# Kernel optimization log

Measured on AMD Instinct MI355X. Metric: run time of the kernel, lower is better.

Reference implementation:

```python
import jax, jax.numpy as jnp
import numpy as np

DIM = 256
HID = DIM * 16

def setup_inputs() -> dict:
    key = jax.random.key(0)
    ks = jax.random.split(key, 6)
    B, L = 4, 2048
    x = jax.random.normal(ks[0], (B, L, DIM), dtype=jnp.float32)
    # nn.Linear(dim, hidden): weight [H, D], bias [H]
    WB = jax.random.normal(ks[1], (HID, DIM), dtype=jnp.float32) / np.sqrt(DIM)
    bB = jax.random.normal(ks[2], (HID,), dtype=jnp.float32) * 0.01
    # nn.Linear(hidden, dim): weight [D, H], bias [D]
    WC = jax.random.normal(ks[3], (DIM, HID), dtype=jnp.float32) / np.sqrt(HID)
    bC = jax.random.normal(ks[4], (DIM,), dtype=jnp.float32) * 0.01
    A = jax.random.normal(ks[5], (HID,), dtype=jnp.float32)
    return {"x": x, "WB": WB, "bB": bB, "WC": WC, "bC": bC, "A": A}

def reference(x, WB, bB, WC, bC, A):
    # b = B(x): [B, L, H]
    b = jnp.einsum('bld,hd->blh', x, WB) + bB
    a = jax.nn.sigmoid(A)  # [H], time-invariant decay
    # h_t = a * h_{t-1} + b_t  (h_0 from zero state) -> associative scan over L
    a_seq = jnp.broadcast_to(a, b.shape)
    def comb(c1, c2):
        a1, u1 = c1
        a2, u2 = c2
        return (a1 * a2, a2 * u1 + u2)
    _, h = jax.lax.associative_scan(comb, (a_seq, b), axis=1)  # [B, L, H]
    # C(h): [B, L, D]
    return jnp.einsum('blh,dh->bld', h, WC) + bC
```

## Files before the change

### kernel.cpp

```cpp
#include <hip/hip_runtime.h>
#include <hip/hip_bf16.h>

#define DIMSZ 256
#define HID 4096
#define BATCH 4
#define SEQ 2048
#define NCH 64
#define CLEN 32
#define SPLITK2 4
#define KCHUNK (HID / SPLITK2)
#define BM2 64

typedef __bf16 bf16_t;
typedef __bf16 bf16x8 __attribute__((ext_vector_type(8)));
typedef float  f32x4  __attribute__((ext_vector_type(4)));

__device__ __forceinline__ float sigmoidf_dev(float x) {
    return 1.0f / (1.0f + __expf(-x));
}

__device__ __forceinline__ void load_lds16(const bf16_t* g, bf16_t* l) {
    __builtin_amdgcn_global_load_lds(
        (const __attribute__((address_space(1))) void*)g,
        (__attribute__((address_space(3))) void*)l,
        16, 0, 0);
}

__device__ __forceinline__ bf16x8 cvt8(const float* p) {
    bf16x8 o;
    #pragma unroll
    for (int j = 0; j < 8; j++) o[j] = (bf16_t)p[j];
    return o;
}

__global__ void prep_kernel(const float* __restrict__ x,
                            const float* __restrict__ WB,
                            const float* __restrict__ WC,
                            bf16_t* __restrict__ xt,
                            bf16_t* __restrict__ WBt,
                            bf16_t* __restrict__ Wt) {
    int i = blockIdx.x * blockDim.x + threadIdx.x;
    if (i < 262144) {
        int lane = i & 63, m16 = (i >> 6) & 511, ks = i >> 15;
        int row = m16 * 16 + (lane & 15);
        int k   = ks * 32 + (lane >> 4) * 8;
        *(bf16x8*)&xt[(size_t)i * 8] = cvt8(&x[(size_t)row * DIMSZ + k]);
    } else if (i < 393216) {
        int j = i - 262144;
        int lane = j & 63, n16 = (j >> 6) & 255, ks = j >> 14;
        int row = n16 * 16 + (lane & 15);
        int k   = ks * 32 + (lane >> 4) * 8;
        *(bf16x8*)&WBt[(size_t)j * 8] = cvt8(&WB[(size_t)row * DIMSZ + k]);
    } else {
        int j = i - 393216;
        int lane = j & 63, g = (j >> 6) & 15, ks = j >> 10;
        int row = g * 16 + (lane & 15);
        int k   = ks * 32 + (lane >> 4) * 8;
        *(bf16x8*)&Wt[(size_t)j * 8] = cvt8(&WC[(size_t)row * HID + k]);
    }
}

__global__ __launch_bounds__(256)
void gemm1_fused(const bf16_t* __restrict__ xt, const bf16_t* __restrict__ WBt,
                 const float* __restrict__ bias, const float* __restrict__ Adecay,
                 bf16_t* __restrict__ Cg, float* __restrict__ totals)
{
    constexpr int N = HID;
    constexpr int LDTILE = 136;
    __shared__ bf16_t tile[128 * LDTILE];

    const int tid = threadIdx.x, wave = tid >> 6, lane = tid & 63;
    const int wm = wave >> 1, wn = wave & 1, q = lane >> 4, r16 = lane & 15;
    const int mBase = blockIdx.x * 128, nBase = blockIdx.y * 128;
    const int m16Base = blockIdx.x * 8 + wm * 4;
    const int n16Base = blockIdx.y * 8 + wn * 4;

    f32x4 acc[4][4] = {};

    #pragma unroll 2
    for (int ks = 0; ks < 8; ks++) {
        bf16x8 af[4], bfr[4];
        #pragma unroll
        for (int mt = 0; mt < 4; mt++)
            af[mt] = *(const bf16x8*)&xt[(((size_t)ks * 512 + m16Base + mt) * 64 + lane) * 8];
        #pragma unroll
        for (int nt = 0; nt < 4; nt++)
            bfr[nt] = *(const bf16x8*)&WBt[(((size_t)ks * 256 + n16Base + nt) * 64 + lane) * 8];
        #pragma unroll
        for (int mt = 0; mt < 4; mt++)
            #pragma unroll
            for (int nt = 0; nt < 4; nt++)
                acc[mt][nt] = __builtin_amdgcn_mfma_f32_16x16x32_bf16(
                    af[mt], bfr[nt], acc[mt][nt], 0, 0, 0);
    }

    #pragma unroll
    for (int nt = 0; nt < 4; nt++) {
        const int chl = wn * 64 + nt * 16 + r16;
        const float bv = bias[nBase + chl];
        #pragma unroll
        for (int mt = 0; mt < 4; mt++) {
            const int t0 = wm * 64 + mt * 16 + q * 4;
            #pragma unroll
            for (int rg = 0; rg < 4; rg++)
                tile[(t0 + rg) * LDTILE + chl] = (bf16_t)(acc[mt][nt][rg] + bv);
        }
    }
    __syncthreads();

    #pragma unroll
    for (int p = 0; p < 8; p++) {
        const int t = p * 16 + (tid >> 4);
        const int ch8 = (tid & 15) << 3;
        *(bf16x8*)&Cg[(size_t)(mBase + t) * N + nBase + ch8] =
            *(const bf16x8*)&tile[t * LDTILE + ch8];
    }

    #pragma unroll
    for (int t = 0; t < 2; t++) {
        int task = tid + t * 256;
        int ch = task & 127, ck = task >> 7;
        float a = sigmoidf_dev(Adecay[nBase + ch]);
        float v[CLEN];
        #pragma unroll
        for (int i = 0; i < CLEN; i++)
            v[i] = (float)tile[(ck * CLEN + i) * LDTILE + ch];
        float tot = 0.f;
        #pragma unroll
        for (int i = 0; i < CLEN; i++)
            tot = a * tot + v[i];
        int batch = mBase >> 11;
        int cg = ((mBase & 2047) >> 5) + ck;
        totals[(size_t)(batch * NCH + cg) * HID + nBase + ch] = tot;
    }
}

__global__ void scan_carries_kernel(const float* __restrict__ totals,
                                    const float* __restrict__ Adecay,
                                    float* __restrict__ carries)
{
    int gid = blockIdx.x * 64 + threadIdx.x;
    int ch    = gid & (HID - 1);
    int batch = gid >> 12;
    float a = sigmoidf_dev(Adecay[ch]);
    float aC = a;
    #pragma unroll
    for (int i = 0; i < 5; i++) aC *= aC;

    float v[NCH];
    #pragma unroll
    for (int c = 0; c < NCH; c++)
        v[c] = totals[(size_t)(batch * NCH + c) * HID + ch];

    float carry = 0.f;
    #pragma unroll
    for (int c = 0; c < NCH; c++) {
        carries[(size_t)(batch * NCH + c) * HID + ch] = carry;
        carry = aC * carry + v[c];
    }
}

__global__ __launch_bounds__(256)
void gemm2_fused(const bf16_t* __restrict__ bv, const bf16_t* __restrict__ Wt,
                 const float* __restrict__ Adecay, const float* __restrict__ carries,
                 bf16_t* __restrict__ P)
{
    constexpr int CKSTRIDE = BM2 * 32 + 32;
    __shared__ bf16_t hs[16896];

    const int tid = threadIdx.x, wave = tid >> 6, lane = tid & 63;
    const int q = lane >> 4, r16 = lane & 15;
    const int mBase = blockIdx.x * BM2;
    const int kBase = blockIdx.y * KCHUNK;
    const int batch = mBase >> 11;
    const int chunk0 = (mBase & 2047) >> 5;

    f32x4 acc[4][4] = {};

    for (int s = 0; s < KCHUNK / 256; s++) {
        const int chSlab = kBase + s * 256;

        if (s > 0) __syncthreads();

        #pragma unroll
        for (int i = 0; i < 8; i++) {
            int ck = wave * 2 + (i >> 2);
            int g  = i & 3;
            load_lds16(&bv[(size_t)(mBase + g * 16 + (lane >> 2)) * HID
                           + chSlab + ck * 32 + ((lane & 3) << 3)],
                       &hs[ck * CKSTRIDE + g * 512]);
        }

        const int ck = tid >> 5, ch = tid & 31;
        const int c = chSlab + ck * 32 + ch;
        const float a = sigmoidf_dev(Adecay[c]);
        float st0 = carries[(size_t)(batch * NCH + chunk0) * HID + c];
        float st1 = carries[(size_t)(batch * NCH + chunk0 + 1) * HID + c];

        __syncthreads();

        {
            bf16_t* hp = &hs[ck * CKSTRIDE + ch];
            float v[BM2];
            #pragma unroll
            for (int t = 0; t < BM2; t++)
                v[t] = (float)hp[t * 32];
            #pragma unroll
            for (int t = 0; t < CLEN; t++) {
                st0 = a * st0 + v[t];
                v[t] = st0;
                st1 = a * st1 + v[t + CLEN];
                v[t + CLEN] = st1;
            }
            #pragma unroll
            for (int t = 0; t < BM2; t++)
                hp[t * 32] = (bf16_t)v[t];
        }
        __syncthreads();

        const int ksBase = (kBase >> 5) + s * 8;
        #pragma unroll 2
        for (int cki = 0; cki < 8; cki++) {
            bf16x8 af[4], bfr[4];
            #pragma unroll
            for (int nt = 0; nt < 4; nt++)
                bfr[nt] = *(const bf16x8*)&Wt[
                    (((size_t)(ksBase + cki) * 16 + wave * 4 + nt) * 64 + lane) * 8];
            #pragma unroll
            for (int mt = 0; mt < 4; mt++)
                af[mt] = *(const bf16x8*)&hs[cki * CKSTRIDE + (mt * 16 + r16) * 32 + q * 8];
            #pragma unroll
            for (int mt = 0; mt < 4; mt++)
                #pragma unroll
                for (int nt = 0; nt < 4; nt++)
                    acc[mt][nt] = __builtin_amdgcn_mfma_f32_16x16x32_bf16(
                        af[mt], bfr[nt], acc[mt][nt], 0, 0, 0);
        }
    }

    __syncthreads();
    #pragma unroll
    for (int nt = 0; nt < 4; nt++) {
        const int col = wave * 64 + nt * 16 + r16;
        #pragma unroll
        for (int mt = 0; mt < 4; mt++)
            #pragma unroll
            for (int rg = 0; rg < 4; rg++)
                hs[(mt * 16 + q * 4 + rg) * 264 + col] = (bf16_t)acc[mt][nt][rg];
    }
    __syncthreads();

    bf16_t* Pb = P + (size_t)blockIdx.y * (BATCH * SEQ) * DIMSZ;
    #pragma unroll
    for (int p = 0; p < 8; p++) {
        int task = p * 256 + tid;
        int r = task >> 5, g8 = (task & 31) << 3;
        *(bf16x8*)&Pb[(size_t)(mBase + r) * DIMSZ + g8] =
            *(const bf16x8*)&hs[r * 264 + g8];
    }
}

__global__ void reduce_out_kernel(const bf16_t* __restrict__ P,
                                  const float* __restrict__ bias,
                                  float* __restrict__ out, int nTask) {
    int i = blockIdx.x * blockDim.x + threadIdx.x;
    if (i >= nTask) return;
    int n8 = (i & 31) << 3;
    size_t off = (size_t)i * 8;
    float v[8];
    #pragma unroll
    for (int j = 0; j < 8; j++) v[j] = bias[n8 + j];
    #pragma unroll
    for (int sp = 0; sp < SPLITK2; sp++) {
        bf16x8 p = *(const bf16x8*)&P[(size_t)sp * (BATCH * SEQ) * DIMSZ + off];
        #pragma unroll
        for (int j = 0; j < 8; j++) v[j] += (float)p[j];
    }
    float4* o4 = (float4*)&out[off];
    o4[0] = make_float4(v[0], v[1], v[2], v[3]);
    o4[1] = make_float4(v[4], v[5], v[6], v[7]);
}

extern "C" void kernel_launch(void* const* d_in, const int* in_sizes, int n_in,
                              void* d_out, int out_size, void* d_ws, size_t ws_size,
                              hipStream_t stream)
{
    const float* x  = (const float*)d_in[0];
    const float* WB = (const float*)d_in[1];
    const float* bB = (const float*)d_in[2];
    const float* WC = (const float*)d_in[3];
    const float* bC = (const float*)d_in[4];
    const float* A  = (const float*)d_in[5];

    char* ws = (char*)d_ws;
    size_t off = 0;
    bf16_t* xt   = (bf16_t*)(ws + off); off += (size_t)BATCH * SEQ * DIMSZ * 2;
    bf16_t* WBt  = (bf16_t*)(ws + off); off += (size_t)HID * DIMSZ * 2;
    bf16_t* Wt   = (bf16_t*)(ws + off); off += (size_t)DIMSZ * HID * 2;
    bf16_t* bbuf = (bf16_t*)(ws + off); off += (size_t)BATCH * SEQ * HID * 2;
    bf16_t* partials = (bf16_t*)(ws + off); off += (size_t)SPLITK2 * BATCH * SEQ * DIMSZ * 2;
    float* totals   = (float*)(ws + off); off += (size_t)BATCH * NCH * HID * 4;
    float* carries  = (float*)(ws + off); off += (size_t)BATCH * NCH * HID * 4;

    const int M = BATCH * SEQ;

    prep_kernel<<<2048, 256, 0, stream>>>(x, WB, WC, xt, WBt, Wt);

    dim3 g1(M / 128, HID / 128);
    gemm1_fused<<<g1, 256, 0, stream>>>(xt, WBt, bB, A, bbuf, totals);

    scan_carries_kernel<<<256, 64, 0, stream>>>(totals, A, carries);

    dim3 g2(M / BM2, SPLITK2);
    gemm2_fused<<<g2, 256, 0, stream>>>(bbuf, Wt, A, carries, partials);

    int nTask = M * DIMSZ / 8;
    reduce_out_kernel<<<(nTask + 255) / 256, 256, 0, stream>>>(
        partials, bC, (float*)d_out, nTask);
}
```

Baseline: 145.2 us.

## Store intermediate B in channel-major layout and prefetch next slab in gemm2

gemm1 now writes its bias-added output transposed (channel-major, time contiguous) through a transposed LDS tile, and computes chunk totals with vectorized 8-wide LDS reads. gemm2 loads time-contiguous rows into a separate staging buffer with a rotated (swizzled) layout, runs the scan from there into the MFMA operand buffer, and issues the next slab's async load right after the scan so it overlaps the MFMA loop. Decay and carry values are hoisted out of the slab loop, and launch bounds request two blocks per CU. This aims to cut strided LDS scan reads and hide global load latency, at the cost of more LDS per block and a layout change that both kernels must agree on.

```diff
diff --git a/kernel.cpp b/kernel.cpp
--- a/kernel.cpp
+++ b/kernel.cpp
@@ -12,6 +12,7 @@
 #define BM2 64
 
 typedef __bf16 bf16_t;
+typedef __bf16 bf16x4 __attribute__((ext_vector_type(4)));
 typedef __bf16 bf16x8 __attribute__((ext_vector_type(8)));
 typedef float  f32x4  __attribute__((ext_vector_type(4)));
 
@@ -65,15 +66,15 @@
                  const float* __restrict__ bias, const float* __restrict__ Adecay,
                  bf16_t* __restrict__ Cg, float* __restrict__ totals)
 {
-    constexpr int N = HID;
-    constexpr int LDTILE = 136;
-    __shared__ bf16_t tile[128 * LDTILE];
+    constexpr int LDT = 136;
+    __shared__ bf16_t tile[128 * LDT];
 
     const int tid = threadIdx.x, wave = tid >> 6, lane = tid & 63;
     const int wm = wave >> 1, wn = wave & 1, q = lane >> 4, r16 = lane & 15;
     const int mBase = blockIdx.x * 128, nBase = blockIdx.y * 128;
     const int m16Base = blockIdx.x * 8 + wm * 4;
     const int n16Base = blockIdx.y * 8 + wn * 4;
+    const int batch = mBase >> 11, tIn = mBase & 2047;
 
     f32x4 acc[4][4] = {};
 
@@ -101,36 +102,37 @@
         #pragma unroll
         for (int mt = 0; mt < 4; mt++) {
             const int t0 = wm * 64 + mt * 16 + q * 4;
+            bf16x4 pk;
             #pragma unroll
             for (int rg = 0; rg < 4; rg++)
-                tile[(t0 + rg) * LDTILE + chl] = (bf16_t)(acc[mt][nt][rg] + bv);
+                pk[rg] = (bf16_t)(acc[mt][nt][rg] + bv);
+            *(bf16x4*)&tile[chl * LDT + t0] = pk;
         }
     }
     __syncthreads();
 
     #pragma unroll
     for (int p = 0; p < 8; p++) {
-        const int t = p * 16 + (tid >> 4);
-        const int ch8 = (tid & 15) << 3;
-        *(bf16x8*)&Cg[(size_t)(mBase + t) * N + nBase + ch8] =
-            *(const bf16x8*)&tile[t * LDTILE + ch8];
+        const int task = p * 256 + tid;
+        const int ch = task >> 4, o = task & 15;
+        *(bf16x8*)&Cg[((size_t)batch * HID + nBase + ch) * SEQ + tIn + o * 8] =
+            *(const bf16x8*)&tile[ch * LDT + o * 8];
     }
 
     #pragma unroll
     for (int t = 0; t < 2; t++) {
-        int task = tid + t * 256;
-        int ch = task & 127, ck = task >> 7;
-        float a = sigmoidf_dev(Adecay[nBase + ch]);
-        float v[CLEN];
-        #pragma unroll
-        for (int i = 0; i < CLEN; i++)
-            v[i] = (float)tile[(ck * CLEN + i) * LDTILE + ch];
+        const int task = tid + t * 256;
+        const int ch = task & 127, ck = task >> 7;
+        const float a = sigmoidf_dev(Adecay[nBase + ch]);
         float tot = 0.f;
         #pragma unroll
-        for (int i = 0; i < CLEN; i++)
-            tot = a * tot + v[i];
-        int batch = mBase >> 11;
-        int cg = ((mBase & 2047) >> 5) + ck;
+        for (int o = 0; o < 4; o++) {
+            bf16x8 v8 = *(const bf16x8*)&tile[ch * LDT + ck * CLEN + o * 8];
+            #pragma unroll
+            for (int j = 0; j < 8; j++)
+                tot = a * tot + (float)v8[j];
+        }
+        const int cg = (tIn >> 5) + ck;
         totals[(size_t)(batch * NCH + cg) * HID + nBase + ch] = tot;
     }
 }
@@ -160,63 +162,79 @@
     }
 }
 
-__global__ __launch_bounds__(256)
+__global__ __launch_bounds__(256, 2)
 void gemm2_fused(const bf16_t* __restrict__ bv, const bf16_t* __restrict__ Wt,
                  const float* __restrict__ Adecay, const float* __restrict__ carries,
                  bf16_t* __restrict__ P)
 {
     constexpr int CKSTRIDE = BM2 * 32 + 32;
     __shared__ bf16_t hs[16896];
+    __shared__ bf16_t hs2[16384];
 
     const int tid = threadIdx.x, wave = tid >> 6, lane = tid & 63;
     const int q = lane >> 4, r16 = lane & 15;
     const int mBase = blockIdx.x * BM2;
     const int kBase = blockIdx.y * KCHUNK;
-    const int batch = mBase >> 11;
-    const int chunk0 = (mBase & 2047) >> 5;
+    const int batch = mBase >> 11, tIn = mBase & 2047;
+    const int chunk0 = tIn >> 5;
+
+    const int srcOct = ((lane & 7) - (lane >> 3)) & 7;
+
+    float aD[4], sd0[4], sd1[4];
+    #pragma unroll
+    for (int s = 0; s < 4; s++) {
+        const int c = kBase + s * 256 + tid;
+        aD[s]  = Adecay[c];
+        sd0[s] = carries[(size_t)(batch * NCH + chunk0) * HID + c];
+        sd1[s] = carries[(size_t)(batch * NCH + chunk0 + 1) * HID + c];
+    }
 
     f32x4 acc[4][4] = {};
 
-    for (int s = 0; s < KCHUNK / 256; s++) {
-        const int chSlab = kBase + s * 256;
-
-        if (s > 0) __syncthreads();
-
+    {
+        const size_t rowBase = (size_t)batch * HID + kBase;
         #pragma unroll
         for (int i = 0; i < 8; i++) {
-            int ck = wave * 2 + (i >> 2);
-            int g  = i & 3;
-            load_lds16(&bv[(size_t)(mBase + g * 16 + (lane >> 2)) * HID
-                           + chSlab + ck * 32 + ((lane & 3) << 3)],
-                       &hs[ck * CKSTRIDE + g * 512]);
-        }
-
-        const int ck = tid >> 5, ch = tid & 31;
-        const int c = chSlab + ck * 32 + ch;
-        const float a = sigmoidf_dev(Adecay[c]);
-        float st0 = carries[(size_t)(batch * NCH + chunk0) * HID + c];
-        float st1 = carries[(size_t)(batch * NCH + chunk0 + 1) * HID + c];
-
+            const int g = wave * 8 + i;
+            load_lds16(&bv[(rowBase + g * 8 + (lane >> 3)) * SEQ + tIn + srcOct * 8],
+                       &hs2[g * 512]);
+        }
+    }
+
+    #pragma unroll
+    for (int s = 0; s < 4; s++) {
         __syncthreads();
 
         {
-            bf16_t* hp = &hs[ck * CKSTRIDE + ch];
-            float v[BM2];
-            #pragma unroll
-            for (int t = 0; t < BM2; t++)
-                v[t] = (float)hp[t * 32];
-            #pragma unroll
-            for (int t = 0; t < CLEN; t++) {
-                st0 = a * st0 + v[t];
-                v[t] = st0;
-                st1 = a * st1 + v[t + CLEN];
-                v[t + CLEN] = st1;
+            const float a = sigmoidf_dev(aD[s]);
+            float st0 = sd0[s], st1 = sd1[s];
+            const int rot = tid & 7;
+            bf16_t* hw = &hs[(tid >> 5) * CKSTRIDE + (tid & 31)];
+            const bf16_t* hr = &hs2[tid * 64];
+            #pragma unroll
+            for (int k = 0; k < 4; k++) {
+                bf16x8 va = *(const bf16x8*)&hr[(((k + rot) & 7)) << 3];
+                bf16x8 vb = *(const bf16x8*)&hr[(((k + 4 + rot) & 7)) << 3];
+                #pragma unroll
+                for (int j = 0; j < 8; j++) {
+                    st0 = a * st0 + (float)va[j];
+                    st1 = a * st1 + (float)vb[j];
+                    hw[(k * 8 + j) * 32]        = (bf16_t)st0;
+                    hw[((k + 4) * 8 + j) * 32]  = (bf16_t)st1;
+                }
             }
-            #pragma unroll
-            for (int t = 0; t < BM2; t++)
-                hp[t * 32] = (bf16_t)v[t];
         }
         __syncthreads();
+
+        if (s < 3) {
+            const size_t rowBase = (size_t)batch * HID + kBase + (s + 1) * 256;
+            #pragma unroll
+            for (int i = 0; i < 8; i++) {
+                const int g = wave * 8 + i;
+                load_lds16(&bv[(rowBase + g * 8 + (lane >> 3)) * SEQ + tIn + srcOct * 8],
+                           &hs2[g * 512]);
+            }
+        }
 
         const int ksBase = (kBase >> 5) + s * 8;
         #pragma unroll 2
```

Result: faster. 141.4 us (-2.6%).
